# Performance work log

Hardware: AMD Instinct MI355X
Metric: run time of the kernel (lower is better)

The kernel has to match this reference:

```python
import jax, jax.numpy as jnp
import numpy as np

E = 8          # num_experts
TOP_K = 2      # num_experts_per_tok
H = 1024       # hidden_size
F = 2048       # intermediate_size
B, S = 2, 4096


def setup_inputs() -> dict:
    key = jax.random.key(0)
    ks = jax.random.split(key, 5)
    hidden_states = jax.random.normal(ks[0], (B, S, H), dtype=jnp.float32)
    gate_w = jax.random.normal(ks[1], (E, H), dtype=jnp.float32) * 0.02   # router: logits = x @ gate_w.T
    Wg = jax.random.normal(ks[2], (E, H, F), dtype=jnp.float32) * 0.02    # gate_proj per expert
    Wu = jax.random.normal(ks[3], (E, H, F), dtype=jnp.float32) * 0.02    # up_proj per expert
    Wd = jax.random.normal(ks[4], (E, F, H), dtype=jnp.float32) * 0.02    # down_proj per expert
    return {"hidden_states": hidden_states, "gate_w": gate_w, "Wg": Wg, "Wu": Wu, "Wd": Wd}


def reference(hidden_states, gate_w, Wg, Wu, Wd):
    b, s, h = hidden_states.shape
    x = hidden_states.reshape(-1, h)                       # [T, H]
    T = x.shape[0]

    router_logits = x @ gate_w.T                           # [T, E]
    probs = jax.nn.softmax(router_logits.astype(jnp.float32), axis=-1)
    topk_w, topk_idx = jax.lax.top_k(probs, TOP_K)         # [T, K]
    topk_w = topk_w / jnp.sum(topk_w, axis=-1, keepdims=True)  # norm_topk_prob
    topk_w = topk_w.astype(x.dtype)

    # Dense per-token-per-expert combine weight (0 for unselected experts).
    w_full = jnp.zeros((T, E), dtype=x.dtype)
    w_full = w_full.at[jnp.arange(T)[:, None], topk_idx].add(topk_w)  # [T, E]

    out = jnp.zeros_like(x)
    for e in range(E):  # fixed small loop over experts
        g = jax.nn.silu(x @ Wg[e]) * (x @ Wu[e])           # [T, F]
        out = out + w_full[:, e:e + 1] * (g @ Wd[e])       # [T, H]

    return out.reshape(b, s, h), router_logits
```

## Files before the change

### kernel.cpp

```cpp
#include <hip/hip_runtime.h>
#include <cstdint>

#define NTOK   8192
#define HDIM   1024
#define FDIM   2048
#define NEXP   8
#define RTOT   (2*NTOK)
#define RPAD   128

typedef unsigned short u16;
typedef short   bf16x8 __attribute__((ext_vector_type(8)));
typedef float   f32x4  __attribute__((ext_vector_type(4)));

__device__ __forceinline__ u16 f2bf(float v) {
  union { float f; uint32_t u; } a; a.f = v;
  uint32_t r = a.u + 0x7FFFu + ((a.u >> 16) & 1u);
  return (u16)(r >> 16);
}

__global__ void router_kernel(const float* __restrict__ x, const float* __restrict__ gw,
                              float* __restrict__ logits, int* __restrict__ te,
                              float* __restrict__ tw) {
  int gid  = blockIdx.x * blockDim.x + threadIdx.x;
  int t    = gid >> 6;
  int lane = gid & 63;
  const float4* xr = (const float4*)(x + (size_t)t * HDIM);
  float acc[NEXP];
#pragma unroll
  for (int e = 0; e < NEXP; ++e) acc[e] = 0.f;
#pragma unroll
  for (int c = 0; c < 4; ++c) {
    float4 xv = xr[c * 64 + lane];
#pragma unroll
    for (int e = 0; e < NEXP; ++e) {
      float4 wv = ((const float4*)(gw + e * HDIM))[c * 64 + lane];
      acc[e] += xv.x * wv.x + xv.y * wv.y + xv.z * wv.z + xv.w * wv.w;
    }
  }
#pragma unroll
  for (int off = 32; off > 0; off >>= 1)
#pragma unroll
    for (int e = 0; e < NEXP; ++e) acc[e] += __shfl_xor(acc[e], off, 64);

  if (lane == 0) {
#pragma unroll
    for (int e = 0; e < NEXP; ++e) logits[(size_t)t * NEXP + e] = acc[e];
    int e1 = 0;
#pragma unroll
    for (int e = 1; e < NEXP; ++e) if (acc[e] > acc[e1]) e1 = e;
    int e2 = -1;
#pragma unroll
    for (int e = 0; e < NEXP; ++e) {
      if (e == e1) continue;
      if (e2 < 0 || acc[e] > acc[e2]) e2 = e;
    }
    float m  = fmaxf(acc[e1], acc[e2]);
    float p1 = __expf(acc[e1] - m), p2 = __expf(acc[e2] - m);
    float inv = 1.f / (p1 + p2);
    te[t * 2]     = e1;  tw[t * 2]     = p1 * inv;
    te[t * 2 + 1] = e2;  tw[t * 2 + 1] = p2 * inv;
  }
}

__global__ void count_kernel(const int* __restrict__ te, int* __restrict__ counts) {
  __shared__ int h[NEXP];
  if (threadIdx.x < NEXP) h[threadIdx.x] = 0;
  __syncthreads();
  const int n = 2 * NTOK;
  for (int i = blockIdx.x * blockDim.x + threadIdx.x; i < n; i += gridDim.x * blockDim.x)
    atomicAdd(&h[te[i]], 1);
  __syncthreads();
  if (threadIdx.x < NEXP) atomicAdd(&counts[threadIdx.x], h[threadIdx.x]);
}

__global__ void prefix_kernel(const int* __restrict__ counts, int* __restrict__ offs,
                              int* __restrict__ cursors) {
  if (threadIdx.x == 0) {
    int s = 0;
    for (int e = 0; e < NEXP; ++e) { offs[e] = s; cursors[e * 16] = s; s += counts[e]; }
    offs[NEXP] = s;
  }
}

__global__ void scatter_kernel(const int* __restrict__ te, const float* __restrict__ tw,
                               int* __restrict__ cursors, int* __restrict__ tok_ids,
                               float* __restrict__ wts) {
  int t    = blockIdx.x * blockDim.x + threadIdx.x;
  int lane = threadIdx.x & 63;
#pragma unroll
  for (int s = 0; s < 2; ++s) {
    int   e = te[t * 2 + s];
    float w = tw[t * 2 + s];
    int pos = 0;
#pragma unroll
    for (int e0 = 0; e0 < NEXP; ++e0) {
      unsigned long long m = __ballot(e == e0);
      if (e == e0) {
        int leader = __ffsll((unsigned long long)m) - 1;
        int rank   = __popcll(m & ((1ull << lane) - 1ull));
        int b = 0;
        if (lane == leader) b = atomicAdd(&cursors[e0 * 16], (int)__popcll(m));
        b = __shfl(b, leader, 64);
        pos = b + rank;
      }
    }
    tok_ids[pos] = t;
    wts[pos] = w;
  }
}

__global__ void gather_cast_kernel(const float* __restrict__ x, const int* __restrict__ tok_ids,
                                   u16* __restrict__ Xg) {
  int j = blockIdx.x;
  int t = tok_ids[j];
  float4 v = ((const float4*)(x + (size_t)t * HDIM))[threadIdx.x];
  ushort4 o;
  o.x = f2bf(v.x); o.y = f2bf(v.y); o.z = f2bf(v.z); o.w = f2bf(v.w);
  ((ushort4*)(Xg + (size_t)j * HDIM))[threadIdx.x] = o;
}

__global__ void transpose_cast_kernel(const float* __restrict__ in, u16* __restrict__ out,
                                      int K, int N) {
  __shared__ float tile[64][65];
  const size_t mat = (size_t)K * N;
  const float* src = in + blockIdx.z * mat + (size_t)(blockIdx.y * 64) * N + blockIdx.x * 64;
  int r = threadIdx.x >> 6;
  int c = threadIdx.x & 63;
#pragma unroll
  for (int i = 0; i < 16; ++i)
    tile[i * 4 + r][c] = src[(size_t)(i * 4 + r) * N + c];
  __syncthreads();
  u16* dst = out + blockIdx.z * mat + (size_t)(blockIdx.x * 64) * K + blockIdx.y * 64;
#pragma unroll
  for (int i = 0; i < 16; ++i) {
    int n = i * 4 + r;
    dst[(size_t)n * K + c] = f2bf(tile[c][n]);
  }
}

__device__ __forceinline__ void stage_tile(const u16* __restrict__ src, int ld,
                                           u16* __restrict__ lds, int wave, int lane) {
#pragma unroll
  for (int i = 0; i < 4; ++i) {
    int chunk = ((i << 2) + wave) << 9;
    int flat  = chunk + (lane << 3);
    int row   = flat >> 6;
    int km    = (flat & 63) ^ ((row & 7) << 3);
    __builtin_amdgcn_global_load_lds(
        (const __attribute__((address_space(1))) uint32_t*)(src + (size_t)row * ld + km),
        (__attribute__((address_space(3))) uint32_t*)(lds + chunk),
        16, 0, 0);
  }
}

__global__ __launch_bounds__(256, 2)
void gemm1_kernel(const u16* __restrict__ Xg, const u16* __restrict__ Wgt,
                  const u16* __restrict__ Wut, const int* __restrict__ offs,
                  u16* __restrict__ G) {
  const int e     = blockIdx.z;
  const int rbase = offs[e];
  const int rows  = offs[e + 1] - rbase;
  const int row0  = blockIdx.y * 128;
  if (row0 >= rows) return;
  const int n0    = blockIdx.x * 128;
  const int arow0 = rbase + row0;

  __shared__ __align__(16) u16 As[128 * 64];
  __shared__ __align__(16) u16 Bgs[128 * 64];
  __shared__ __align__(16) u16 Bus[128 * 64];

  const int tid  = threadIdx.x;
  const int wave = tid >> 6;
  const int lane = tid & 63;
  const int wm   = wave >> 1, wn = wave & 1;
  const int l15  = lane & 15, quad = lane >> 4;

  const u16* Ag = Xg  + (size_t)arow0 * HDIM;
  const u16* Bg = Wgt + (size_t)e * FDIM * HDIM + (size_t)n0 * HDIM;
  const u16* Bu = Wut + (size_t)e * FDIM * HDIM + (size_t)n0 * HDIM;

  f32x4 accg[4][4], accu[4][4];
#pragma unroll
  for (int i = 0; i < 4; ++i)
#pragma unroll
    for (int j = 0; j < 4; ++j) { accg[i][j] = (f32x4)0.f; accu[i][j] = (f32x4)0.f; }

  for (int kt = 0; kt < HDIM / 64; ++kt) {
    const int k0 = kt * 64;
    stage_tile(Ag + k0, HDIM, As,  wave, lane);
    stage_tile(Bg + k0, HDIM, Bgs, wave, lane);
    stage_tile(Bu + k0, HDIM, Bus, wave, lane);
    __syncthreads();
#pragma unroll
    for (int kk = 0; kk < 64; kk += 32) {
      bf16x8 af[4];
#pragma unroll
      for (int im = 0; im < 4; ++im) {
        int r  = wm * 64 + im * 16 + l15;
        int kq = (kk + quad * 8) ^ ((r & 7) << 3);
        af[im] = *(const bf16x8*)(As + r * 64 + kq);
      }
#pragma unroll
      for (int in = 0; in < 4; ++in) {
        int r  = wn * 64 + in * 16 + l15;
        int kq = (kk + quad * 8) ^ ((r & 7) << 3);
        bf16x8 bg = *(const bf16x8*)(Bgs + r * 64 + kq);
        bf16x8 bu = *(const bf16x8*)(Bus + r * 64 + kq);
#pragma unroll
        for (int im = 0; im < 4; ++im) {
          accg[im][in] = __builtin_amdgcn_mfma_f32_16x16x32_bf16(af[im], bg, accg[im][in], 0, 0, 0);
          accu[im][in] = __builtin_amdgcn_mfma_f32_16x16x32_bf16(af[im], bu, accu[im][in], 0, 0, 0);
        }
      }
    }
    __syncthreads();
  }

#pragma unroll
  for (int im = 0; im < 4; ++im) {
#pragma unroll
    for (int rr = 0; rr < 4; ++rr) {
      int lrow = row0 + wm * 64 + im * 16 + quad * 4 + rr;
      if (lrow < rows) {
        size_t grow = (size_t)(rbase + lrow);
#pragma unroll
        for (int in = 0; in < 4; ++in) {
          float g = accg[im][in][rr];
          float u = accu[im][in][rr];
          float val = g / (1.f + __expf(-g)) * u;
          int gcol = n0 + wn * 64 + in * 16 + l15;
          G[grow * FDIM + gcol] = f2bf(val);
        }
      }
    }
  }
}

__global__ __launch_bounds__(256, 2)
void gemm2_kernel(const u16* __restrict__ G, const u16* __restrict__ Wdt,
                  const int* __restrict__ offs, const int* __restrict__ tok_ids,
                  const float* __restrict__ wts, float* __restrict__ out) {
  const int e     = blockIdx.z;
  const int rbase = offs[e];
  const int rows  = offs[e + 1] - rbase;
  const int row0  = blockIdx.y * 128;
  if (row0 >= rows) return;
  const int n0    = blockIdx.x * 128;
  const int arow0 = rbase + row0;

  __shared__ __align__(16) u16 As[128 * 64];
  __shared__ __align__(16) u16 Bs[128 * 64];

  const int tid  = threadIdx.x;
  const int wave = tid >> 6;
  const int lane = tid & 63;
  const int wm   = wave >> 1, wn = wave & 1;
  const int l15  = lane & 15, quad = lane >> 4;

  const u16* Ag = G   + (size_t)arow0 * FDIM;
  const u16* Bg = Wdt + (size_t)e * HDIM * FDIM + (size_t)n0 * FDIM;

  f32x4 acc[4][4];
#pragma unroll
  for (int i = 0; i < 4; ++i)
#pragma unroll
    for (int j = 0; j < 4; ++j) acc[i][j] = (f32x4)0.f;

  for (int kt = 0; kt < FDIM / 64; ++kt) {
    const int k0 = kt * 64;
    stage_tile(Ag + k0, FDIM, As, wave, lane);
    stage_tile(Bg + k0, FDIM, Bs, wave, lane);
    __syncthreads();
#pragma unroll
    for (int kk = 0; kk < 64; kk += 32) {
      bf16x8 af[4], bf[4];
#pragma unroll
      for (int im = 0; im < 4; ++im) {
        int r  = wm * 64 + im * 16 + l15;
        int kq = (kk + quad * 8) ^ ((r & 7) << 3);
        af[im] = *(const bf16x8*)(As + r * 64 + kq);
      }
#pragma unroll
      for (int in = 0; in < 4; ++in) {
        int r  = wn * 64 + in * 16 + l15;
        int kq = (kk + quad * 8) ^ ((r & 7) << 3);
        bf[in] = *(const bf16x8*)(Bs + r * 64 + kq);
      }
#pragma unroll
      for (int in = 0; in < 4; ++in)
#pragma unroll
        for (int im = 0; im < 4; ++im)
          acc[im][in] = __builtin_amdgcn_mfma_f32_16x16x32_bf16(af[im], bf[in], acc[im][in], 0, 0, 0);
    }
    __syncthreads();
  }

#pragma unroll
  for (int im = 0; im < 4; ++im) {
#pragma unroll
    for (int rr = 0; rr < 4; ++rr) {
      int lrow = row0 + wm * 64 + im * 16 + quad * 4 + rr;
      if (lrow < rows) {
        int grow = rbase + lrow;
        int t    = tok_ids[grow];
        float w  = wts[grow];
        float* orow = out + (size_t)t * HDIM + n0 + wn * 64 + l15;
#pragma unroll
        for (int in = 0; in < 4; ++in)
          unsafeAtomicAdd(orow + in * 16, acc[im][in][rr] * w);
      }
    }
  }
}

extern "C" void kernel_launch(void* const* d_in, const int* in_sizes, int n_in,
                              void* d_out, int out_size, void* d_ws, size_t ws_size,
                              hipStream_t stream) {
  const float* x  = (const float*)d_in[0];
  const float* gw = (const float*)d_in[1];
  const float* Wg = (const float*)d_in[2];
  const float* Wu = (const float*)d_in[3];
  const float* Wd = (const float*)d_in[4];

  float* out    = (float*)d_out;
  float* logits = out + (size_t)NTOK * HDIM;

  char* p = (char*)d_ws;
  u16* Wgt = (u16*)p;  p += (size_t)NEXP * FDIM * HDIM * 2;
  u16* Wut = (u16*)p;  p += (size_t)NEXP * FDIM * HDIM * 2;
  u16* Wdt = (u16*)p;  p += (size_t)NEXP * HDIM * FDIM * 2;
  u16* Xg  = (u16*)p;  p += (size_t)(RTOT + RPAD) * HDIM * 2;
  u16* G   = (u16*)p;  p += (size_t)(RTOT + RPAD) * FDIM * 2;
  int*   tok_ids = (int*)p;   p += (RTOT + RPAD) * 4;
  float* wts     = (float*)p; p += (RTOT + RPAD) * 4;
  int*   te      = (int*)p;   p += NTOK * 2 * 4;
  float* tw      = (float*)p; p += NTOK * 2 * 4;
  int*   counts  = (int*)p;   p += NEXP * 4;
  int*   offs    = (int*)p;   p += (NEXP + 1) * 4;
  int*   cursors = (int*)p;   p += NEXP * 16 * 4;

  hipMemsetAsync(out, 0, (size_t)NTOK * HDIM * sizeof(float), stream);
  hipMemsetAsync(counts, 0, NEXP * sizeof(int), stream);

  router_kernel<<<(NTOK * 64) / 256, 256, 0, stream>>>(x, gw, logits, te, tw);
  count_kernel<<<16, 256, 0, stream>>>(te, counts);
  prefix_kernel<<<1, 64, 0, stream>>>(counts, offs, cursors);
  scatter_kernel<<<NTOK / 256, 256, 0, stream>>>(te, tw, cursors, tok_ids, wts);
  gather_cast_kernel<<<RTOT, 256, 0, stream>>>(x, tok_ids, Xg);

  transpose_cast_kernel<<<dim3(FDIM / 64, HDIM / 64, NEXP), 256, 0, stream>>>(Wg, Wgt, HDIM, FDIM);
  transpose_cast_kernel<<<dim3(FDIM / 64, HDIM / 64, NEXP), 256, 0, stream>>>(Wu, Wut, HDIM, FDIM);
  transpose_cast_kernel<<<dim3(HDIM / 64, FDIM / 64, NEXP), 256, 0, stream>>>(Wd, Wdt, FDIM, HDIM);

  gemm1_kernel<<<dim3(FDIM / 128, 64, NEXP), 256, 0, stream>>>(Xg, Wgt, Wut, offs, G);
  gemm2_kernel<<<dim3(HDIM / 128, 64, NEXP), 256, 0, stream>>>(G, Wdt, offs, tok_ids, wts, out);
}
```

Before: 568.2 us.

## Replace atomic combine with slot-indexed bf16 output plus combine kernel; fuse prep kernels

The down-projection now writes weighted bf16 rows into a per-slot buffer that reuses the gathered-input storage, instead of atomically adding fp32 into the output. A new combine kernel sums each token's two slots, which removes the output memset and the atomic traffic. Counting and prefix sum are merged into one single-block kernel, and the three weight transpose/cast kernels become one launch with float4 loads and 16-byte packed stores. The cost is an extra pass over Y and bf16 rounding of each expert's contribution before the sum.

```diff
diff --git a/kernel.cpp b/kernel.cpp
--- a/kernel.cpp
+++ b/kernel.cpp
@@ -11,11 +11,15 @@
 typedef unsigned short u16;
 typedef short   bf16x8 __attribute__((ext_vector_type(8)));
 typedef float   f32x4  __attribute__((ext_vector_type(4)));
+typedef u16     u16x8  __attribute__((ext_vector_type(8)));
 
 __device__ __forceinline__ u16 f2bf(float v) {
   union { float f; uint32_t u; } a; a.f = v;
   uint32_t r = a.u + 0x7FFFu + ((a.u >> 16) & 1u);
   return (u16)(r >> 16);
+}
+__device__ __forceinline__ float bf2f(u16 b) {
+  union { uint32_t u; float f; } a; a.u = ((uint32_t)b) << 16; return a.f;
 }
 
 __global__ void router_kernel(const float* __restrict__ x, const float* __restrict__ gw,
@@ -62,29 +66,40 @@
   }
 }
 
-__global__ void count_kernel(const int* __restrict__ te, int* __restrict__ counts) {
-  __shared__ int h[NEXP];
-  if (threadIdx.x < NEXP) h[threadIdx.x] = 0;
+__global__ void count_prefix_kernel(const int* __restrict__ te, int* __restrict__ offs,
+                                    int* __restrict__ cursors) {
+  __shared__ int wsum[16][NEXP];
+  int cnt[NEXP];
+#pragma unroll
+  for (int e = 0; e < NEXP; ++e) cnt[e] = 0;
+  for (int i = threadIdx.x; i < 2 * NTOK; i += 1024) {
+    int v = te[i];
+#pragma unroll
+    for (int e = 0; e < NEXP; ++e) cnt[e] += (v == e) ? 1 : 0;
+  }
+#pragma unroll
+  for (int off = 32; off > 0; off >>= 1)
+#pragma unroll
+    for (int e = 0; e < NEXP; ++e) cnt[e] += __shfl_xor(cnt[e], off, 64);
+  int wave = threadIdx.x >> 6, lane = threadIdx.x & 63;
+  if (lane == 0)
+#pragma unroll
+    for (int e = 0; e < NEXP; ++e) wsum[wave][e] = cnt[e];
   __syncthreads();
-  const int n = 2 * NTOK;
-  for (int i = blockIdx.x * blockDim.x + threadIdx.x; i < n; i += gridDim.x * blockDim.x)
-    atomicAdd(&h[te[i]], 1);
-  __syncthreads();
-  if (threadIdx.x < NEXP) atomicAdd(&counts[threadIdx.x], h[threadIdx.x]);
-}
-
-__global__ void prefix_kernel(const int* __restrict__ counts, int* __restrict__ offs,
-                              int* __restrict__ cursors) {
   if (threadIdx.x == 0) {
     int s = 0;
-    for (int e = 0; e < NEXP; ++e) { offs[e] = s; cursors[e * 16] = s; s += counts[e]; }
+    for (int e = 0; e < NEXP; ++e) {
+      int c = 0;
+      for (int w = 0; w < 16; ++w) c += wsum[w][e];
+      offs[e] = s; cursors[e * 16] = s; s += c;
+    }
     offs[NEXP] = s;
   }
 }
 
 __global__ void scatter_kernel(const int* __restrict__ te, const float* __restrict__ tw,
                                int* __restrict__ cursors, int* __restrict__ tok_ids,
-                               float* __restrict__ wts) {
+                               float* __restrict__ wts, int* __restrict__ slots) {
   int t    = blockIdx.x * blockDim.x + threadIdx.x;
   int lane = threadIdx.x & 63;
 #pragma unroll
@@ -106,6 +121,7 @@
     }
     tok_ids[pos] = t;
     wts[pos] = w;
+    slots[t * 2 + s] = pos;
   }
 }
 
@@ -119,22 +135,44 @@
   ((ushort4*)(Xg + (size_t)j * HDIM))[threadIdx.x] = o;
 }
 
-__global__ void transpose_cast_kernel(const float* __restrict__ in, u16* __restrict__ out,
-                                      int K, int N) {
-  __shared__ float tile[64][65];
-  const size_t mat = (size_t)K * N;
-  const float* src = in + blockIdx.z * mat + (size_t)(blockIdx.y * 64) * N + blockIdx.x * 64;
-  int r = threadIdx.x >> 6;
-  int c = threadIdx.x & 63;
-#pragma unroll
-  for (int i = 0; i < 16; ++i)
-    tile[i * 4 + r][c] = src[(size_t)(i * 4 + r) * N + c];
+__global__ __launch_bounds__(256)
+void prep_weights_kernel(const float* __restrict__ Wg, const float* __restrict__ Wu,
+                         const float* __restrict__ Wd, u16* __restrict__ Wgt,
+                         u16* __restrict__ Wut, u16* __restrict__ Wdt) {
+  __shared__ float tile[64 * 65];
+  const int mat = blockIdx.z >> 3;
+  const int e   = blockIdx.z & 7;
+  const int K   = (mat < 2) ? HDIM : FDIM;
+  const int N   = (mat < 2) ? FDIM : HDIM;
+  const float* src = ((mat == 0) ? Wg : (mat == 1) ? Wu : Wd) + (size_t)e * K * N;
+  u16*         dst = ((mat == 0) ? Wgt : (mat == 1) ? Wut : Wdt) + (size_t)e * K * N;
+  const int tn = (mat < 2) ? blockIdx.x : blockIdx.y;
+  const int tk = (mat < 2) ? blockIdx.y : blockIdx.x;
+  const int k0 = tk * 64, n0 = tn * 64;
+
+  const int r  = threadIdx.x >> 2;
+  const int c4 = threadIdx.x & 3;
+#pragma unroll
+  for (int i = 0; i < 4; ++i) {
+    int c = (c4 + i * 4) * 4;
+    float4 v = *(const float4*)(src + (size_t)(k0 + r) * N + n0 + c);
+    tile[r * 65 + c]     = v.x;
+    tile[r * 65 + c + 1] = v.y;
+    tile[r * 65 + c + 2] = v.z;
+    tile[r * 65 + c + 3] = v.w;
+  }
   __syncthreads();
-  u16* dst = out + blockIdx.z * mat + (size_t)(blockIdx.x * 64) * K + blockIdx.y * 64;
-#pragma unroll
-  for (int i = 0; i < 16; ++i) {
-    int n = i * 4 + r;
-    dst[(size_t)n * K + c] = f2bf(tile[c][n]);
+
+  const int kq = threadIdx.x & 7;
+  const int nr = threadIdx.x >> 3;
+#pragma unroll
+  for (int p = 0; p < 2; ++p) {
+    int n = p * 32 + nr;
+    u16x8 pk;
+#pragma unroll
+    for (int j = 0; j < 8; ++j)
+      pk[j] = f2bf(tile[(kq * 8 + j) * 65 + n]);
+    *(u16x8*)(dst + (size_t)(n0 + n) * K + k0 + kq * 8) = pk;
   }
 }
 
@@ -238,8 +276,8 @@
 
 __global__ __launch_bounds__(256, 2)
 void gemm2_kernel(const u16* __restrict__ G, const u16* __restrict__ Wdt,
-                  const int* __restrict__ offs, const int* __restrict__ tok_ids,
-                  const float* __restrict__ wts, float* __restrict__ out) {
+                  const int* __restrict__ offs, const float* __restrict__ wts,
+                  u16* __restrict__ Y) {
   const int e     = blockIdx.z;
   const int rbase = offs[e];
   const int rows  = offs[e + 1] - rbase;
@@ -302,15 +340,28 @@
       int lrow = row0 + wm * 64 + im * 16 + quad * 4 + rr;
       if (lrow < rows) {
         int grow = rbase + lrow;
-        int t    = tok_ids[grow];
         float w  = wts[grow];
-        float* orow = out + (size_t)t * HDIM + n0 + wn * 64 + l15;
+        u16* yrow = Y + (size_t)grow * HDIM + n0 + wn * 64 + l15;
 #pragma unroll
         for (int in = 0; in < 4; ++in)
-          unsafeAtomicAdd(orow + in * 16, acc[im][in][rr] * w);
-      }
-    }
-  }
+          yrow[in * 16] = f2bf(acc[im][in][rr] * w);
+      }
+    }
+  }
+}
+
+__global__ void combine_kernel(const u16* __restrict__ Y, const int* __restrict__ slots,
+                               float* __restrict__ out) {
+  int t  = blockIdx.x;
+  int s1 = slots[2 * t], s2 = slots[2 * t + 1];
+  ushort4 a = ((const ushort4*)(Y + (size_t)s1 * HDIM))[threadIdx.x];
+  ushort4 b = ((const ushort4*)(Y + (size_t)s2 * HDIM))[threadIdx.x];
+  float4 o;
+  o.x = bf2f(a.x) + bf2f(b.x);
+  o.y = bf2f(a.y) + bf2f(b.y);
+  o.z = bf2f(a.z) + bf2f(b.z);
+  o.w = bf2f(a.w) + bf2f(b.w);
+  ((float4*)(out + (size_t)t * HDIM))[threadIdx.x] = o;
 }
 
 extern "C" void kernel_launch(void* const* d_in, const int* in_sizes, int n_in,
@@ -335,23 +386,20 @@
   float* wts     = (float*)p; p += (RTOT + RPAD) * 4;
   int*   te      = (int*)p;   p += NTOK * 2 * 4;
   float* tw      = (float*)p; p += NTOK * 2 * 4;
-  int*   counts  = (int*)p;   p += NEXP * 4;
+  int*   slots   = (int*)p;   p += NTOK * 2 * 4;
   int*   offs    = (int*)p;   p += (NEXP + 1) * 4;
   int*   cursors = (int*)p;   p += NEXP * 16 * 4;
 
-  hipMemsetAsync(out, 0, (size_t)NTOK * HDIM * sizeof(float), stream);
-  hipMemsetAsync(counts, 0, NEXP * sizeof(int), stream);
+  u16* Y = Xg;
 
   router_kernel<<<(NTOK * 64) / 256, 256, 0, stream>>>(x, gw, logits, te, tw);
-  count_kernel<<<16, 256, 0, stream>>>(te, counts);
-  prefix_kernel<<<1, 64, 0, stream>>>(counts, offs, cursors);
-  scatter_kernel<<<NTOK / 256, 256, 0, stream>>>(te, tw, cursors, tok_ids, wts);
+  count_prefix_kernel<<<1, 1024, 0, stream>>>(te, offs, cursors);
+  scatter_kernel<<<NTOK / 256, 256, 0, stream>>>(te, tw, cursors, tok_ids, wts, slots);
   gather_cast_kernel<<<RTOT, 256, 0, stream>>>(x, tok_ids, Xg);
 
-  transpose_cast_kernel<<<dim3(FDIM / 64, HDIM / 64, NEXP), 256, 0, stream>>>(Wg, Wgt, HDIM, FDIM);
-  transpose_cast_kernel<<<dim3(FDIM / 64, HDIM / 64, NEXP), 256, 0, stream>>>(Wu, Wut, HDIM, FDIM);
-  transpose_cast_kernel<<<dim3(HDIM / 64, FDIM / 64, NEXP), 256, 0, stream>>>(Wd, Wdt, FDIM, HDIM);
+  prep_weights_kernel<<<dim3(32, 16, 24), 256, 0, stream>>>(Wg, Wu, Wd, Wgt, Wut, Wdt);
 
   gemm1_kernel<<<dim3(FDIM / 128, 64, NEXP), 256, 0, stream>>>(Xg, Wgt, Wut, offs, G);
-  gemm2_kernel<<<dim3(HDIM / 128, 64, NEXP), 256, 0, stream>>>(G, Wdt, offs, tok_ids, wts, out);
-}
+  gemm2_kernel<<<dim3(HDIM / 128, 64, NEXP), 256, 0, stream>>>(G, Wdt, offs, wts, Y);
+  combine_kernel<<<NTOK, 256, 0, stream>>>(Y, slots, out);
+}
```

Result: faster. 556.3 us (-2.1%).
